# Performance work log

Hardware: AMD Instinct MI355X
Metric: run time of the kernel (lower is better)

The kernel has to match this reference:

```python
import jax, jax.numpy as jnp
import numpy as np

N_NODES = 10000
N_EDGES = 640000
D = 128


def setup_inputs() -> dict:
    key = jax.random.key(0)
    ks = jax.random.split(key, 8)
    x = jax.random.normal(ks[0], (N_NODES, D), dtype=jnp.float32)
    edge_weight = jax.random.uniform(ks[1], (N_EDGES,), dtype=jnp.float32)
    W0 = jax.random.normal(ks[2], (D, D), dtype=jnp.float32) * (1.0 / np.sqrt(D))
    b0 = jnp.zeros((D,), dtype=jnp.float32)
    W1 = jax.random.normal(ks[3], (D, D), dtype=jnp.float32) * (1.0 / np.sqrt(D))
    b1 = jnp.zeros((D,), dtype=jnp.float32)
    src = jax.random.randint(ks[4], (N_EDGES,), 0, N_NODES)
    dst = jax.random.randint(ks[5], (N_EDGES,), 0, N_NODES)
    return {"x": x, "edge_weight": edge_weight, "W0": W0, "b0": b0,
            "W1": W1, "b1": b1, "src": src, "dst": dst}


def _graph_conv(h, src, dst, edge_weight, W, b):
    # DGL GraphConv with norm='both', bias, activation=relu.
    n = h.shape[0]
    ones = jnp.ones((src.shape[0],), dtype=h.dtype)
    out_deg = jax.ops.segment_sum(ones, src, num_segments=n)
    in_deg = jax.ops.segment_sum(ones, dst, num_segments=n)
    norm_src = jax.lax.rsqrt(jnp.maximum(out_deg, 1.0))  # [N]
    norm_dst = jax.lax.rsqrt(jnp.maximum(in_deg, 1.0))   # [N]
    h = h * norm_src[:, None]
    # gather -> weight edges -> scatter-add (sparse neighbor aggregation)
    msg = h[src] * edge_weight[:, None]                  # [E, D]
    agg = jax.ops.segment_sum(msg, dst, num_segments=n)  # [N, D]
    rst = agg @ W                                        # in_feats == out_feats: aggregate first
    rst = rst * norm_dst[:, None] + b
    return jax.nn.relu(rst)  # activation inside GraphConv


def reference(x, edge_weight, W0, b0, W1, b1, src, dst):
    # NET.forward (full-graph path): per layer GraphConv -> activation -> dropout.
    # Dropout is identity in eval mode; outer relu after GraphConv's internal relu is idempotent
    # but applied for faithfulness.
    h = jax.nn.relu(_graph_conv(x, src, dst, edge_weight, W0, b0))
    h = jax.nn.relu(_graph_conv(h, src, dst, edge_weight, W1, b1))
    return h  # predict is None (n_classes=None)
```

## Files before the change

kernel.cpp:

```cpp
#include <hip/hip_runtime.h>
#include <hip/hip_fp16.h>

#define D 128
#define NB 256
#define Q 8
#define BQ (NB / Q)
#define NBINS_MAX 10016
#define GM 32

__global__ __launch_bounds__(256) void hist_kernel(const int* __restrict__ src, const int* __restrict__ dst,
                                                   const float* __restrict__ x, __half* __restrict__ xh, int total4,
                                                   int* __restrict__ pd, unsigned short* __restrict__ ps,
                                                   int E, int n) {
    __shared__ __align__(16) int hd[NBINS_MAX];
    __shared__ __align__(16) int hs[NBINS_MAX];
    int b = blockIdx.x, t = threadIdx.x;
    for (int i = b * 256 + t; i < total4; i += NB * 256) {
        float4 v = *(const float4*)(x + (size_t)i * 4);
        __half2 a = __floats2half2_rn(v.x, v.y);
        __half2 c = __floats2half2_rn(v.z, v.w);
        *(__half2*)(xh + (size_t)i * 4) = a;
        *(__half2*)(xh + (size_t)i * 4 + 2) = c;
    }
    int chunk = (E + NB - 1) / NB;
    int e0 = b * chunk, e1 = min(e0 + chunk, E);
    int nq = (n + 3) >> 2;
    for (int i = t; i < nq; i += 256) {
        *(int4*)(&hd[i * 4]) = make_int4(0, 0, 0, 0);
        *(int4*)(&hs[i * 4]) = make_int4(0, 0, 0, 0);
    }
    __syncthreads();
    for (int e = e0 + t; e < e1; e += 256) {
        atomicAdd(&hd[dst[e]], 1);
        atomicAdd(&hs[src[e]], 1);
    }
    __syncthreads();
    int nf = n >> 2;
    for (int i = t; i < nf; i += 256) {
        int4 h = *(const int4*)(&hd[i * 4]);
        *(int4*)(pd + (size_t)b * n + i * 4) = h;
        int4 s = *(const int4*)(&hs[i * 4]);
        uint2 u;
        u.x = (unsigned)(s.x & 0xFFFF) | ((unsigned)(s.y & 0xFFFF) << 16);
        u.y = (unsigned)(s.z & 0xFFFF) | ((unsigned)(s.w & 0xFFFF) << 16);
        *(uint2*)(ps + (size_t)b * n + i * 4) = u;
    }
    for (int i = nf * 4 + t; i < n; i += 256) {
        pd[(size_t)b * n + i] = hd[i];
        ps[(size_t)b * n + i] = (unsigned short)hs[i];
    }
}

__global__ __launch_bounds__(256) void colscan_kernel(int* __restrict__ pd, const unsigned short* __restrict__ ps,
                                                      int* __restrict__ qtot_d, int* __restrict__ qtot_s, int n) {
    int bin4 = (blockIdx.x * 256 + threadIdx.x) * 4;
    int q = blockIdx.y;
    if (bin4 >= n) return;
    int b0 = q * BQ;
    if (bin4 + 3 < n) {
        int4 run = make_int4(0, 0, 0, 0);
        int4 ssum = make_int4(0, 0, 0, 0);
#pragma unroll 8
        for (int j = 0; j < BQ; ++j) {
            size_t idx = (size_t)(b0 + j) * n + bin4;
            int4 v = *(const int4*)(pd + idx);
            *(int4*)(pd + idx) = run;
            run.x += v.x; run.y += v.y; run.z += v.z; run.w += v.w;
            uint2 u = *(const uint2*)(ps + idx);
            ssum.x += (int)(u.x & 0xFFFF); ssum.y += (int)(u.x >> 16);
            ssum.z += (int)(u.y & 0xFFFF); ssum.w += (int)(u.y >> 16);
        }
        *(int4*)(qtot_d + (size_t)q * n + bin4) = run;
        *(int4*)(qtot_s + (size_t)q * n + bin4) = ssum;
    } else {
        for (int bin = bin4; bin < n; ++bin) {
            int run = 0, ssum = 0;
            for (int j = 0; j < BQ; ++j) {
                size_t idx = (size_t)(b0 + j) * n + bin;
                int v = pd[idx];
                pd[idx] = run;
                run += v;
                ssum += (int)ps[idx];
            }
            qtot_d[(size_t)q * n + bin] = run;
            qtot_s[(size_t)q * n + bin] = ssum;
        }
    }
}

__global__ __launch_bounds__(1024) void finscan_kernel(int* __restrict__ qtot_d, const int* __restrict__ qtot_s,
                                                       int* __restrict__ row_start,
                                                       float* __restrict__ norm_src, float* __restrict__ norm_dst,
                                                       int n) {
    __shared__ int deg[NBINS_MAX];
    __shared__ int part[1024];
    int t = threadIdx.x;
    for (int b4 = t * 4; b4 < n; b4 += 4096) {
        if (b4 + 3 < n) {
            int4 qv[Q];
#pragma unroll
            for (int q = 0; q < Q; ++q) qv[q] = *(const int4*)(qtot_d + (size_t)q * n + b4);
            int4 run = make_int4(0, 0, 0, 0);
#pragma unroll
            for (int q = 0; q < Q; ++q) {
                *(int4*)(qtot_d + (size_t)q * n + b4) = run;
                run.x += qv[q].x; run.y += qv[q].y; run.z += qv[q].z; run.w += qv[q].w;
            }
            *(int4*)(&deg[b4]) = run;
            norm_dst[b4 + 0] = rsqrtf(fmaxf((float)run.x, 1.0f));
            norm_dst[b4 + 1] = rsqrtf(fmaxf((float)run.y, 1.0f));
            norm_dst[b4 + 2] = rsqrtf(fmaxf((float)run.z, 1.0f));
            norm_dst[b4 + 3] = rsqrtf(fmaxf((float)run.w, 1.0f));
            int4 st = make_int4(0, 0, 0, 0);
#pragma unroll
            for (int q = 0; q < Q; ++q) {
                int4 v = *(const int4*)(qtot_s + (size_t)q * n + b4);
                st.x += v.x; st.y += v.y; st.z += v.z; st.w += v.w;
            }
            norm_src[b4 + 0] = rsqrtf(fmaxf((float)st.x, 1.0f));
            norm_src[b4 + 1] = rsqrtf(fmaxf((float)st.y, 1.0f));
            norm_src[b4 + 2] = rsqrtf(fmaxf((float)st.z, 1.0f));
            norm_src[b4 + 3] = rsqrtf(fmaxf((float)st.w, 1.0f));
        } else {
            for (int bin = b4; bin < n; ++bin) {
                int run = 0;
                for (int q = 0; q < Q; ++q) {
                    size_t i = (size_t)q * n + bin;
                    int v = qtot_d[i];
                    qtot_d[i] = run;
                    run += v;
                }
                deg[bin] = run;
                norm_dst[bin] = rsqrtf(fmaxf((float)run, 1.0f));
                int tot = 0;
                for (int q = 0; q < Q; ++q) tot += qtot_s[(size_t)q * n + bin];
                norm_src[bin] = rsqrtf(fmaxf((float)tot, 1.0f));
            }
        }
    }
    __syncthreads();
    int ipt = (n + 1023) / 1024;
    int lo = min(t * ipt, n), hi = min(lo + ipt, n);
    int s = 0;
    for (int i = lo; i < hi; ++i) s += deg[i];
    part[t] = s;
    __syncthreads();
    for (int off = 1; off < 1024; off <<= 1) {
        int v = 0;
        if (t >= off) v = part[t - off];
        __syncthreads();
        if (t >= off) part[t] += v;
        __syncthreads();
    }
    int run = part[t] - s;
    for (int i = lo; i < hi; ++i) {
        int v = deg[i];
        row_start[i] = run;
        run += v;
    }
    if (t == 1023) row_start[n] = part[1023];
}

__global__ __launch_bounds__(256) void fill_kernel(const int* __restrict__ src, const int* __restrict__ dst,
                                                   const float* __restrict__ ew, const float* __restrict__ ns,
                                                   const int* __restrict__ row_start, const int* __restrict__ qbase,
                                                   const int* __restrict__ pd,
                                                   int2* __restrict__ sorted, int E, int n) {
    __shared__ __align__(16) int cursor[NBINS_MAX];
    int b = blockIdx.x, t = threadIdx.x;
    int q = b / BQ;
    int chunk = (E + NB - 1) / NB;
    int e0 = b * chunk, e1 = min(e0 + chunk, E);
    int nf = n >> 2;
    for (int i = t; i < nf; i += 256) {
        int4 r = *(const int4*)(row_start + i * 4);
        int4 a = *(const int4*)(qbase + (size_t)q * n + i * 4);
        int4 c = *(const int4*)(pd + (size_t)b * n + i * 4);
        *(int4*)(&cursor[i * 4]) = make_int4(r.x + a.x + c.x, r.y + a.y + c.y,
                                             r.z + a.z + c.z, r.w + a.w + c.w);
    }
    for (int i = nf * 4 + t; i < n; i += 256)
        cursor[i] = row_start[i] + qbase[(size_t)q * n + i] + pd[(size_t)b * n + i];
    __syncthreads();
    for (int e = e0 + t; e < e1; e += 256) {
        int d = dst[e];
        int slot = atomicAdd(&cursor[d], 1);
        int s = src[e];
        int2 rec;
        rec.x = s;
        rec.y = __float_as_int(ew[e] * ns[s]);
        sorted[slot] = rec;
    }
}

template <int EPI>
__global__ __launch_bounds__(256) void agg_kernel(const __half* __restrict__ h, const int* __restrict__ row_start,
                                                  const int2* __restrict__ sorted, float* __restrict__ out,
                                                  const float* __restrict__ norm_dst, const float* __restrict__ bias,
                                                  int n) {
    int wave = threadIdx.x >> 6;
    int lane = threadIdx.x & 63;
    int node = blockIdx.x * 4 + wave;
    if (node >= n) return;
    const __half2* hc = (const __half2*)h + lane;
    int beg = __builtin_amdgcn_readfirstlane(row_start[node]);
    int end = __builtin_amdgcn_readfirstlane(row_start[node + 1]);
    float accx = 0.f, accy = 0.f;
    int s = beg;
    if (s < end && (s & 1)) {
        int2 rr = sorted[s];
        float w = __int_as_float(rr.y);
        float2 f = __half22float2(hc[(size_t)rr.x << 6]);
        accx = fmaf(w, f.x, accx); accy = fmaf(w, f.y, accy);
        ++s;
    }
    int4 p0, p1, p2, p3, p4, p5, p6, p7;
    if (s + 16 <= end) {
        p0 = *(const int4*)(sorted + s);
        p1 = *(const int4*)(sorted + s + 2);
        p2 = *(const int4*)(sorted + s + 4);
        p3 = *(const int4*)(sorted + s + 6);
        p4 = *(const int4*)(sorted + s + 8);
        p5 = *(const int4*)(sorted + s + 10);
        p6 = *(const int4*)(sorted + s + 12);
        p7 = *(const int4*)(sorted + s + 14);
    }
    for (; s + 32 <= end; s += 16) {
        int4 q0 = *(const int4*)(sorted + s + 16);
        int4 q1 = *(const int4*)(sorted + s + 18);
        int4 q2 = *(const int4*)(sorted + s + 20);
        int4 q3 = *(const int4*)(sorted + s + 22);
        int4 q4 = *(const int4*)(sorted + s + 24);
        int4 q5 = *(const int4*)(sorted + s + 26);
        int4 q6 = *(const int4*)(sorted + s + 28);
        int4 q7 = *(const int4*)(sorted + s + 30);
        __half2 x0  = hc[(size_t)p0.x << 6];
        __half2 x1  = hc[(size_t)p0.z << 6];
        __half2 x2  = hc[(size_t)p1.x << 6];
        __half2 x3  = hc[(size_t)p1.z << 6];
        __half2 x4  = hc[(size_t)p2.x << 6];
        __half2 x5  = hc[(size_t)p2.z << 6];
        __half2 x6  = hc[(size_t)p3.x << 6];
        __half2 x7  = hc[(size_t)p3.z << 6];
        __half2 x8  = hc[(size_t)p4.x << 6];
        __half2 x9  = hc[(size_t)p4.z << 6];
        __half2 x10 = hc[(size_t)p5.x << 6];
        __half2 x11 = hc[(size_t)p5.z << 6];
        __half2 x12 = hc[(size_t)p6.x << 6];
        __half2 x13 = hc[(size_t)p6.z << 6];
        __half2 x14 = hc[(size_t)p7.x << 6];
        __half2 x15 = hc[(size_t)p7.z << 6];
        float2 f;
        f = __half22float2(x0);  accx = fmaf(__int_as_float(p0.y), f.x, accx); accy = fmaf(__int_as_float(p0.y), f.y, accy);
        f = __half22float2(x1);  accx = fmaf(__int_as_float(p0.w), f.x, accx); accy = fmaf(__int_as_float(p0.w), f.y, accy);
        f = __half22float2(x2);  accx = fmaf(__int_as_float(p1.y), f.x, accx); accy = fmaf(__int_as_float(p1.y), f.y, accy);
        f = __half22float2(x3);  accx = fmaf(__int_as_float(p1.w), f.x, accx); accy = fmaf(__int_as_float(p1.w), f.y, accy);
        f = __half22float2(x4);  accx = fmaf(__int_as_float(p2.y), f.x, accx); accy = fmaf(__int_as_float(p2.y), f.y, accy);
        f = __half22float2(x5);  accx = fmaf(__int_as_float(p2.w), f.x, accx); accy = fmaf(__int_as_float(p2.w), f.y, accy);
        f = __half22float2(x6);  accx = fmaf(__int_as_float(p3.y), f.x, accx); accy = fmaf(__int_as_float(p3.y), f.y, accy);
        f = __half22float2(x7);  accx = fmaf(__int_as_float(p3.w), f.x, accx); accy = fmaf(__int_as_float(p3.w), f.y, accy);
        f = __half22float2(x8);  accx = fmaf(__int_as_float(p4.y), f.x, accx); accy = fmaf(__int_as_float(p4.y), f.y, accy);
        f = __half22float2(x9);  accx = fmaf(__int_as_float(p4.w), f.x, accx); accy = fmaf(__int_as_float(p4.w), f.y, accy);
        f = __half22float2(x10); accx = fmaf(__int_as_float(p5.y), f.x, accx); accy = fmaf(__int_as_float(p5.y), f.y, accy);
        f = __half22float2(x11); accx = fmaf(__int_as_float(p5.w), f.x, accx); accy = fmaf(__int_as_float(p5.w), f.y, accy);
        f = __half22float2(x12); accx = fmaf(__int_as_float(p6.y), f.x, accx); accy = fmaf(__int_as_float(p6.y), f.y, accy);
        f = __half22float2(x13); accx = fmaf(__int_as_float(p6.w), f.x, accx); accy = fmaf(__int_as_float(p6.w), f.y, accy);
        f = __half22float2(x14); accx = fmaf(__int_as_float(p7.y), f.x, accx); accy = fmaf(__int_as_float(p7.y), f.y, accy);
        f = __half22float2(x15); accx = fmaf(__int_as_float(p7.w), f.x, accx); accy = fmaf(__int_as_float(p7.w), f.y, accy);
        p0 = q0; p1 = q1; p2 = q2; p3 = q3;
        p4 = q4; p5 = q5; p6 = q6; p7 = q7;
    }
    if (s + 16 <= end) {
        float2 f;
        f = __half22float2(hc[(size_t)p0.x << 6]); accx = fmaf(__int_as_float(p0.y), f.x, accx); accy = fmaf(__int_as_float(p0.y), f.y, accy);
        f = __half22float2(hc[(size_t)p0.z << 6]); accx = fmaf(__int_as_float(p0.w), f.x, accx); accy = fmaf(__int_as_float(p0.w), f.y, accy);
        f = __half22float2(hc[(size_t)p1.x << 6]); accx = fmaf(__int_as_float(p1.y), f.x, accx); accy = fmaf(__int_as_float(p1.y), f.y, accy);
        f = __half22float2(hc[(size_t)p1.z << 6]); accx = fmaf(__int_as_float(p1.w), f.x, accx); accy = fmaf(__int_as_float(p1.w), f.y, accy);
        f = __half22float2(hc[(size_t)p2.x << 6]); accx = fmaf(__int_as_float(p2.y), f.x, accx); accy = fmaf(__int_as_float(p2.y), f.y, accy);
        f = __half22float2(hc[(size_t)p2.z << 6]); accx = fmaf(__int_as_float(p2.w), f.x, accx); accy = fmaf(__int_as_float(p2.w), f.y, accy);
        f = __half22float2(hc[(size_t)p3.x << 6]); accx = fmaf(__int_as_float(p3.y), f.x, accx); accy = fmaf(__int_as_float(p3.y), f.y, accy);
        f = __half22float2(hc[(size_t)p3.z << 6]); accx = fmaf(__int_as_float(p3.w), f.x, accx); accy = fmaf(__int_as_float(p3.w), f.y, accy);
        f = __half22float2(hc[(size_t)p4.x << 6]); accx = fmaf(__int_as_float(p4.y), f.x, accx); accy = fmaf(__int_as_float(p4.y), f.y, accy);
        f = __half22float2(hc[(size_t)p4.z << 6]); accx = fmaf(__int_as_float(p4.w), f.x, accx); accy = fmaf(__int_as_float(p4.w), f.y, accy);
        f = __half22float2(hc[(size_t)p5.x << 6]); accx = fmaf(__int_as_float(p5.y), f.x, accx); accy = fmaf(__int_as_float(p5.y), f.y, accy);
        f = __half22float2(hc[(size_t)p5.z << 6]); accx = fmaf(__int_as_float(p5.w), f.x, accx); accy = fmaf(__int_as_float(p5.w), f.y, accy);
        f = __half22float2(hc[(size_t)p6.x << 6]); accx = fmaf(__int_as_float(p6.y), f.x, accx); accy = fmaf(__int_as_float(p6.y), f.y, accy);
        f = __half22float2(hc[(size_t)p6.z << 6]); accx = fmaf(__int_as_float(p6.w), f.x, accx); accy = fmaf(__int_as_float(p6.w), f.y, accy);
        f = __half22float2(hc[(size_t)p7.x << 6]); accx = fmaf(__int_as_float(p7.y), f.x, accx); accy = fmaf(__int_as_float(p7.y), f.y, accy);
        f = __half22float2(hc[(size_t)p7.z << 6]); accx = fmaf(__int_as_float(p7.w), f.x, accx); accy = fmaf(__int_as_float(p7.w), f.y, accy);
        s += 16;
    }
    if (s + 8 <= end) {
        int4 a0 = *(const int4*)(sorted + s);
        int4 a1 = *(const int4*)(sorted + s + 2);
        int4 a2 = *(const int4*)(sorted + s + 4);
        int4 a3 = *(const int4*)(sorted + s + 6);
        float2 f;
        f = __half22float2(hc[(size_t)a0.x << 6]); accx = fmaf(__int_as_float(a0.y), f.x, accx); accy = fmaf(__int_as_float(a0.y), f.y, accy);
        f = __half22float2(hc[(size_t)a0.z << 6]); accx = fmaf(__int_as_float(a0.w), f.x, accx); accy = fmaf(__int_as_float(a0.w), f.y, accy);
        f = __half22float2(hc[(size_t)a1.x << 6]); accx = fmaf(__int_as_float(a1.y), f.x, accx); accy = fmaf(__int_as_float(a1.y), f.y, accy);
        f = __half22float2(hc[(size_t)a1.z << 6]); accx = fmaf(__int_as_float(a1.w), f.x, accx); accy = fmaf(__int_as_float(a1.w), f.y, accy);
        f = __half22float2(hc[(size_t)a2.x << 6]); accx = fmaf(__int_as_float(a2.y), f.x, accx); accy = fmaf(__int_as_float(a2.y), f.y, accy);
        f = __half22float2(hc[(size_t)a2.z << 6]); accx = fmaf(__int_as_float(a2.w), f.x, accx); accy = fmaf(__int_as_float(a2.w), f.y, accy);
        f = __half22float2(hc[(size_t)a3.x << 6]); accx = fmaf(__int_as_float(a3.y), f.x, accx); accy = fmaf(__int_as_float(a3.y), f.y, accy);
        f = __half22float2(hc[(size_t)a3.z << 6]); accx = fmaf(__int_as_float(a3.w), f.x, accx); accy = fmaf(__int_as_float(a3.w), f.y, accy);
        s += 8;
    }
    for (; s + 2 <= end; s += 2) {
        int4 p = *(const int4*)(sorted + s);
        float2 f;
        f = __half22float2(hc[(size_t)p.x << 6]); accx = fmaf(__int_as_float(p.y), f.x, accx); accy = fmaf(__int_as_float(p.y), f.y, accy);
        f = __half22float2(hc[(size_t)p.z << 6]); accx = fmaf(__int_as_float(p.w), f.x, accx); accy = fmaf(__int_as_float(p.w), f.y, accy);
    }
    if (s < end) {
        int2 rr = sorted[s];
        float w = __int_as_float(rr.y);
        float2 f = __half22float2(hc[(size_t)rr.x << 6]);
        accx = fmaf(w, f.x, accx); accy = fmaf(w, f.y, accy);
    }
    float2 o;
    if (EPI) {
        float nd = norm_dst[node];
        o.x = fmaxf(fmaf(accx, nd, bias[lane * 2]), 0.f);
        o.y = fmaxf(fmaf(accy, nd, bias[lane * 2 + 1]), 0.f);
    } else {
        o.x = accx; o.y = accy;
    }
    *(float2*)(out + ((size_t)node << 7) + lane * 2) = o;
}

__global__ __launch_bounds__(256) void gemmfused_kernel(const float* __restrict__ A,
                                                        const float* __restrict__ W0, const float* __restrict__ b0,
                                                        const float* __restrict__ W1,
                                                        const float* __restrict__ norm_dst,
                                                        __half* __restrict__ out_h, int n) {
    __shared__ __align__(16) float sAT[D][GM + 2];
    int tid = threadIdx.x;
    int row0 = blockIdx.x * GM;
    for (int i = tid; i < GM * 32; i += 256) {
        int r = i >> 5;
        int kq = i & 31;
        int rr = row0 + r;
        float4 v = make_float4(0.f, 0.f, 0.f, 0.f);
        if (rr < n) v = *(const float4*)(A + (size_t)rr * D + kq * 4);
        sAT[kq * 4 + 0][r] = v.x;
        sAT[kq * 4 + 1][r] = v.y;
        sAT[kq * 4 + 2][r] = v.z;
        sAT[kq * 4 + 3][r] = v.w;
    }
    __syncthreads();
    int tx = tid & 15;
    int ty = tid >> 4;
    int c0 = tx * 8;
    int r0 = ty * 2;
    float acc0[8], acc1[8];
#pragma unroll
    for (int j = 0; j < 8; ++j) { acc0[j] = 0.f; acc1[j] = 0.f; }
    {
        const float* Wk = W0 + c0;
#pragma unroll 4
        for (int k = 0; k < D; ++k) {
            float2 a = *(const float2*)&sAT[k][r0];
            float4 w0 = *(const float4*)(Wk);
            float4 w1 = *(const float4*)(Wk + 4);
            Wk += D;
            acc0[0] = fmaf(a.x, w0.x, acc0[0]);
            acc0[1] = fmaf(a.x, w0.y, acc0[1]);
            acc0[2] = fmaf(a.x, w0.z, acc0[2]);
            acc0[3] = fmaf(a.x, w0.w, acc0[3]);
            acc0[4] = fmaf(a.x, w1.x, acc0[4]);
            acc0[5] = fmaf(a.x, w1.y, acc0[5]);
            acc0[6] = fmaf(a.x, w1.z, acc0[6]);
            acc0[7] = fmaf(a.x, w1.w, acc0[7]);
            acc1[0] = fmaf(a.y, w0.x, acc1[0]);
            acc1[1] = fmaf(a.y, w0.y, acc1[1]);
            acc1[2] = fmaf(a.y, w0.z, acc1[2]);
            acc1[3] = fmaf(a.y, w0.w, acc1[3]);
            acc1[4] = fmaf(a.y, w1.x, acc1[4]);
            acc1[5] = fmaf(a.y, w1.y, acc1[5]);
            acc1[6] = fmaf(a.y, w1.z, acc1[6]);
            acc1[7] = fmaf(a.y, w1.w, acc1[7]);
        }
    }
    __syncthreads();
#pragma unroll 2
    for (int rr = 0; rr < 2; ++rr) {
        int r = row0 + r0 + rr;
        if (r >= n) continue;
        float* acc = rr ? acc1 : acc0;
        float nd = norm_dst[r];
#pragma unroll
        for (int j = 0; j < 8; ++j)
            sAT[c0 + j][r0 + rr] = fmaxf(fmaf(acc[j], nd, b0[c0 + j]), 0.f);
    }
    __syncthreads();
#pragma unroll
    for (int j = 0; j < 8; ++j) { acc0[j] = 0.f; acc1[j] = 0.f; }
    {
        const float* Wk = W1 + c0;
#pragma unroll 4
        for (int k = 0; k < D; ++k) {
            float2 a = *(const float2*)&sAT[k][r0];
            float4 w0 = *(const float4*)(Wk);
            float4 w1 = *(const float4*)(Wk + 4);
            Wk += D;
            acc0[0] = fmaf(a.x, w0.x, acc0[0]);
            acc0[1] = fmaf(a.x, w0.y, acc0[1]);
            acc0[2] = fmaf(a.x, w0.z, acc0[2]);
            acc0[3] = fmaf(a.x, w0.w, acc0[3]);
            acc0[4] = fmaf(a.x, w1.x, acc0[4]);
            acc0[5] = fmaf(a.x, w1.y, acc0[5]);
            acc0[6] = fmaf(a.x, w1.z, acc0[6]);
            acc0[7] = fmaf(a.x, w1.w, acc0[7]);
            acc1[0] = fmaf(a.y, w0.x, acc1[0]);
            acc1[1] = fmaf(a.y, w0.y, acc1[1]);
            acc1[2] = fmaf(a.y, w0.z, acc1[2]);
            acc1[3] = fmaf(a.y, w0.w, acc1[3]);
            acc1[4] = fmaf(a.y, w1.x, acc1[4]);
            acc1[5] = fmaf(a.y, w1.y, acc1[5]);
            acc1[6] = fmaf(a.y, w1.z, acc1[6]);
            acc1[7] = fmaf(a.y, w1.w, acc1[7]);
        }
    }
#pragma unroll 2
    for (int rr = 0; rr < 2; ++rr) {
        int r = row0 + r0 + rr;
        if (r >= n) continue;
        float* acc = rr ? acc1 : acc0;
        __half2 h0 = __floats2half2_rn(acc[0], acc[1]);
        __half2 h1 = __floats2half2_rn(acc[2], acc[3]);
        __half2 h2 = __floats2half2_rn(acc[4], acc[5]);
        __half2 h3 = __floats2half2_rn(acc[6], acc[7]);
        __half* p = out_h + (size_t)r * D + c0;
        *(__half2*)(p + 0) = h0;
        *(__half2*)(p + 2) = h1;
        *(__half2*)(p + 4) = h2;
        *(__half2*)(p + 6) = h3;
    }
}

extern "C" void kernel_launch(void* const* d_in, const int* in_sizes, int n_in,
                              void* d_out, int out_size, void* d_ws, size_t ws_size,
                              hipStream_t stream) {
    const float* x  = (const float*)d_in[0];
    const float* ew = (const float*)d_in[1];
    const float* W0 = (const float*)d_in[2];
    const float* b0 = (const float*)d_in[3];
    const float* W1 = (const float*)d_in[4];
    const float* b1 = (const float*)d_in[5];
    const int* src  = (const int*)d_in[6];
    const int* dst  = (const int*)d_in[7];
    float* out = (float*)d_out;

    int n = in_sizes[0] / D;
    int E = in_sizes[6];
    if (n <= 0 || E <= 0) return;

    char* ws = (char*)d_ws;
    size_t off = 0;
    auto alloc = [&](size_t bytes) -> void* {
        void* p = ws + off;
        off = (off + bytes + 255) & ~(size_t)255;
        return p;
    };
    int* row_start  = (int*)alloc(((size_t)n + 1) * 4);
    float* norm_src = (float*)alloc((size_t)n * 4);
    float* norm_dst = (float*)alloc((size_t)n * 4);
    int* qtot_d     = (int*)alloc((size_t)Q * n * 4);
    int* qtot_s     = (int*)alloc((size_t)Q * n * 4);
    int2* sorted    = (int2*)alloc((size_t)E * 8);
    int* pd         = (int*)alloc((size_t)NB * n * 4);
    unsigned short* ps = (unsigned short*)alloc((size_t)NB * n * 2);
    float* B1       = (float*)alloc((size_t)n * D * 4);
    __half* xh      = (__half*)alloc((size_t)n * D * 2);
    __half* th      = (__half*)alloc((size_t)n * D * 2);

    int nb4 = (n + 1023) / 1024;
    int ab = (n + 3) / 4;
    int gb = (n + GM - 1) / GM;

    hist_kernel<<<NB, 256, 0, stream>>>(src, dst, x, xh, n * D / 4, pd, ps, E, n);
    colscan_kernel<<<dim3(nb4, Q), 256, 0, stream>>>(pd, ps, qtot_d, qtot_s, n);
    finscan_kernel<<<1, 1024, 0, stream>>>(qtot_d, qtot_s, row_start, norm_src, norm_dst, n);
    fill_kernel<<<NB, 256, 0, stream>>>(src, dst, ew, norm_src, row_start, qtot_d, pd, sorted, E, n);

    agg_kernel<0><<<ab, 256, 0, stream>>>(xh, row_start, sorted, B1, nullptr, nullptr, n);
    gemmfused_kernel<<<gb, 256, 0, stream>>>(B1, W0, b0, W1, norm_dst, th, n);
    agg_kernel<1><<<ab, 256, 0, stream>>>(th, row_start, sorted, out, norm_dst, b1, n);
}
```

Baseline: 182.4 us.

## Fuse CSR preprocessing kernels into one persistent kernel with grid barriers

Merges the histogram, column-scan, final-scan and fill kernels into a single persistent kernel of NB blocks separated by software grid barriers built on atomic counters. The single-block 1024-thread final scan becomes a multi-block scan with per-block partial sums and a serial base computation. This is meant to remove three kernel launch gaps and the serial single-block scan bottleneck. It relies on all 256 blocks being co-resident, which large shared memory use makes a deadlock risk if occupancy is insufficient, and it adds a memset plus spin-wait costs.

```diff
diff --git a/kernel.cpp b/kernel.cpp
--- a/kernel.cpp
+++ b/kernel.cpp
@@ -8,13 +8,35 @@
 #define NBINS_MAX 10016
 #define GM 32
 
-__global__ __launch_bounds__(256) void hist_kernel(const int* __restrict__ src, const int* __restrict__ dst,
-                                                   const float* __restrict__ x, __half* __restrict__ xh, int total4,
-                                                   int* __restrict__ pd, unsigned short* __restrict__ ps,
-                                                   int E, int n) {
+__device__ __forceinline__ void gridbar(int* bar, int phase) {
+    __syncthreads();
+    if (threadIdx.x == 0) {
+        __threadfence();
+        atomicAdd(bar, 1);
+        int target = NB * (phase + 1);
+        while (atomicAdd(bar, 0) < target) { __builtin_amdgcn_s_sleep(2); }
+        __threadfence();
+    }
+    __syncthreads();
+}
+
+__global__ __launch_bounds__(256) void preprocess_kernel(
+        const int* __restrict__ src, const int* __restrict__ dst,
+        const float* __restrict__ x, __half* __restrict__ xh, int total4,
+        const float* __restrict__ ew,
+        int* __restrict__ pd, unsigned short* __restrict__ ps,
+        int* __restrict__ qtot_d, int* __restrict__ qtot_s,
+        int* __restrict__ row_start, float* __restrict__ norm_src, float* __restrict__ norm_dst,
+        int2* __restrict__ sorted,
+        int* __restrict__ bar, int* __restrict__ part_g, int* __restrict__ base_g,
+        int E, int n, int nb4) {
     __shared__ __align__(16) int hd[NBINS_MAX];
     __shared__ __align__(16) int hs[NBINS_MAX];
     int b = blockIdx.x, t = threadIdx.x;
+    int chunk = (E + NB - 1) / NB;
+    int e0 = b * chunk, e1 = min(e0 + chunk, E);
+    int nf = n >> 2;
+
     for (int i = b * 256 + t; i < total4; i += NB * 256) {
         float4 v = *(const float4*)(x + (size_t)i * 4);
         __half2 a = __floats2half2_rn(v.x, v.y);
@@ -22,8 +44,6 @@
         *(__half2*)(xh + (size_t)i * 4) = a;
         *(__half2*)(xh + (size_t)i * 4 + 2) = c;
     }
-    int chunk = (E + NB - 1) / NB;
-    int e0 = b * chunk, e1 = min(e0 + chunk, E);
     int nq = (n + 3) >> 2;
     for (int i = t; i < nq; i += 256) {
         *(int4*)(&hd[i * 4]) = make_int4(0, 0, 0, 0);
@@ -35,7 +55,6 @@
         atomicAdd(&hs[src[e]], 1);
     }
     __syncthreads();
-    int nf = n >> 2;
     for (int i = t; i < nf; i += 256) {
         int4 h = *(const int4*)(&hd[i * 4]);
         *(int4*)(pd + (size_t)b * n + i * 4) = h;
@@ -49,54 +68,55 @@
         pd[(size_t)b * n + i] = hd[i];
         ps[(size_t)b * n + i] = (unsigned short)hs[i];
     }
-}
-
-__global__ __launch_bounds__(256) void colscan_kernel(int* __restrict__ pd, const unsigned short* __restrict__ ps,
-                                                      int* __restrict__ qtot_d, int* __restrict__ qtot_s, int n) {
-    int bin4 = (blockIdx.x * 256 + threadIdx.x) * 4;
-    int q = blockIdx.y;
-    if (bin4 >= n) return;
-    int b0 = q * BQ;
-    if (bin4 + 3 < n) {
-        int4 run = make_int4(0, 0, 0, 0);
-        int4 ssum = make_int4(0, 0, 0, 0);
+    gridbar(bar, 0);
+
+    if (b < nb4 * Q) {
+        int gx = b % nb4;
+        int q  = b / nb4;
+        int bin4 = (gx * 256 + t) * 4;
+        if (bin4 < n) {
+            int b0 = q * BQ;
+            if (bin4 + 3 < n) {
+                int4 run = make_int4(0, 0, 0, 0);
+                int4 ssum = make_int4(0, 0, 0, 0);
 #pragma unroll 8
-        for (int j = 0; j < BQ; ++j) {
-            size_t idx = (size_t)(b0 + j) * n + bin4;
-            int4 v = *(const int4*)(pd + idx);
-            *(int4*)(pd + idx) = run;
-            run.x += v.x; run.y += v.y; run.z += v.z; run.w += v.w;
-            uint2 u = *(const uint2*)(ps + idx);
-            ssum.x += (int)(u.x & 0xFFFF); ssum.y += (int)(u.x >> 16);
-            ssum.z += (int)(u.y & 0xFFFF); ssum.w += (int)(u.y >> 16);
-        }
-        *(int4*)(qtot_d + (size_t)q * n + bin4) = run;
-        *(int4*)(qtot_s + (size_t)q * n + bin4) = ssum;
-    } else {
-        for (int bin = bin4; bin < n; ++bin) {
-            int run = 0, ssum = 0;
-            for (int j = 0; j < BQ; ++j) {
-                size_t idx = (size_t)(b0 + j) * n + bin;
-                int v = pd[idx];
-                pd[idx] = run;
-                run += v;
-                ssum += (int)ps[idx];
+                for (int j = 0; j < BQ; ++j) {
+                    size_t idx = (size_t)(b0 + j) * n + bin4;
+                    int4 v = *(const int4*)(pd + idx);
+                    *(int4*)(pd + idx) = run;
+                    run.x += v.x; run.y += v.y; run.z += v.z; run.w += v.w;
+                    uint2 u = *(const uint2*)(ps + idx);
+                    ssum.x += (int)(u.x & 0xFFFF); ssum.y += (int)(u.x >> 16);
+                    ssum.z += (int)(u.y & 0xFFFF); ssum.w += (int)(u.y >> 16);
+                }
+                *(int4*)(qtot_d + (size_t)q * n + bin4) = run;
+                *(int4*)(qtot_s + (size_t)q * n + bin4) = ssum;
+            } else {
+                for (int bin = bin4; bin < n; ++bin) {
+                    int run = 0, ssum = 0;
+                    for (int j = 0; j < BQ; ++j) {
+                        size_t idx = (size_t)(b0 + j) * n + bin;
+                        int v = pd[idx];
+                        pd[idx] = run;
+                        run += v;
+                        ssum += (int)ps[idx];
+                    }
+                    qtot_d[(size_t)q * n + bin] = run;
+                    qtot_s[(size_t)q * n + bin] = ssum;
+                }
             }
-            qtot_d[(size_t)q * n + bin] = run;
-            qtot_s[(size_t)q * n + bin] = ssum;
-        }
-    }
-}
-
-__global__ __launch_bounds__(1024) void finscan_kernel(int* __restrict__ qtot_d, const int* __restrict__ qtot_s,
-                                                       int* __restrict__ row_start,
-                                                       float* __restrict__ norm_src, float* __restrict__ norm_dst,
-                                                       int n) {
-    __shared__ int deg[NBINS_MAX];
-    __shared__ int part[1024];
-    int t = threadIdx.x;
-    for (int b4 = t * 4; b4 < n; b4 += 4096) {
-        if (b4 + 3 < n) {
+        }
+    }
+    gridbar(bar, 1);
+
+    int* degL = hs;
+    int* redL = hd;
+    if (b < nb4) {
+        int l4 = t * 4;
+        int b4 = b * 1024 + l4;
+        int cnt = (b4 < n) ? min(4, n - b4) : 0;
+        int tot = 0;
+        if (cnt == 4) {
             int4 qv[Q];
 #pragma unroll
             for (int q = 0; q < Q; ++q) qv[q] = *(const int4*)(qtot_d + (size_t)q * n + b4);
@@ -106,7 +126,7 @@
                 *(int4*)(qtot_d + (size_t)q * n + b4) = run;
                 run.x += qv[q].x; run.y += qv[q].y; run.z += qv[q].z; run.w += qv[q].w;
             }
-            *(int4*)(&deg[b4]) = run;
+            *(int4*)(&degL[l4]) = run;
             norm_dst[b4 + 0] = rsqrtf(fmaxf((float)run.x, 1.0f));
             norm_dst[b4 + 1] = rsqrtf(fmaxf((float)run.y, 1.0f));
             norm_dst[b4 + 2] = rsqrtf(fmaxf((float)run.z, 1.0f));
@@ -121,8 +141,10 @@
             norm_src[b4 + 1] = rsqrtf(fmaxf((float)st.y, 1.0f));
             norm_src[b4 + 2] = rsqrtf(fmaxf((float)st.z, 1.0f));
             norm_src[b4 + 3] = rsqrtf(fmaxf((float)st.w, 1.0f));
-        } else {
-            for (int bin = b4; bin < n; ++bin) {
+            tot = run.x + run.y + run.z + run.w;
+        } else if (cnt > 0) {
+            for (int j = 0; j < cnt; ++j) {
+                int bin = b4 + j;
                 int run = 0;
                 for (int q = 0; q < Q; ++q) {
                     size_t i = (size_t)q * n + bin;
@@ -130,66 +152,78 @@
                     qtot_d[i] = run;
                     run += v;
                 }
-                deg[bin] = run;
+                degL[l4 + j] = run;
+                tot += run;
                 norm_dst[bin] = rsqrtf(fmaxf((float)run, 1.0f));
-                int tot = 0;
-                for (int q = 0; q < Q; ++q) tot += qtot_s[(size_t)q * n + bin];
-                norm_src[bin] = rsqrtf(fmaxf((float)tot, 1.0f));
+                int tt = 0;
+                for (int q = 0; q < Q; ++q) tt += qtot_s[(size_t)q * n + bin];
+                norm_src[bin] = rsqrtf(fmaxf((float)tt, 1.0f));
             }
         }
-    }
-    __syncthreads();
-    int ipt = (n + 1023) / 1024;
-    int lo = min(t * ipt, n), hi = min(lo + ipt, n);
-    int s = 0;
-    for (int i = lo; i < hi; ++i) s += deg[i];
-    part[t] = s;
-    __syncthreads();
-    for (int off = 1; off < 1024; off <<= 1) {
-        int v = 0;
-        if (t >= off) v = part[t - off];
+        redL[t] = tot;
         __syncthreads();
-        if (t >= off) part[t] += v;
+        for (int off = 128; off > 0; off >>= 1) {
+            if (t < off) redL[t] += redL[t + off];
+            __syncthreads();
+        }
+        if (t == 0) part_g[b] = redL[0];
+    }
+    gridbar(bar, 2);
+
+    if (b == 0 && t == 0) {
+        int running = 0;
+        for (int i = 0; i < nb4; ++i) {
+            base_g[i] = running;
+            running += part_g[i];
+        }
+        row_start[n] = running;
+    }
+    gridbar(bar, 3);
+
+    if (b < nb4) {
+        int l4 = t * 4;
+        int b4 = b * 1024 + l4;
+        int cnt = (b4 < n) ? min(4, n - b4) : 0;
+        int tot = 0;
+        for (int j = 0; j < cnt; ++j) tot += degL[l4 + j];
+        redL[t] = tot;
         __syncthreads();
-    }
-    int run = part[t] - s;
-    for (int i = lo; i < hi; ++i) {
-        int v = deg[i];
-        row_start[i] = run;
-        run += v;
-    }
-    if (t == 1023) row_start[n] = part[1023];
-}
-
-__global__ __launch_bounds__(256) void fill_kernel(const int* __restrict__ src, const int* __restrict__ dst,
-                                                   const float* __restrict__ ew, const float* __restrict__ ns,
-                                                   const int* __restrict__ row_start, const int* __restrict__ qbase,
-                                                   const int* __restrict__ pd,
-                                                   int2* __restrict__ sorted, int E, int n) {
-    __shared__ __align__(16) int cursor[NBINS_MAX];
-    int b = blockIdx.x, t = threadIdx.x;
-    int q = b / BQ;
-    int chunk = (E + NB - 1) / NB;
-    int e0 = b * chunk, e1 = min(e0 + chunk, E);
-    int nf = n >> 2;
-    for (int i = t; i < nf; i += 256) {
-        int4 r = *(const int4*)(row_start + i * 4);
-        int4 a = *(const int4*)(qbase + (size_t)q * n + i * 4);
-        int4 c = *(const int4*)(pd + (size_t)b * n + i * 4);
-        *(int4*)(&cursor[i * 4]) = make_int4(r.x + a.x + c.x, r.y + a.y + c.y,
-                                             r.z + a.z + c.z, r.w + a.w + c.w);
-    }
-    for (int i = nf * 4 + t; i < n; i += 256)
-        cursor[i] = row_start[i] + qbase[(size_t)q * n + i] + pd[(size_t)b * n + i];
-    __syncthreads();
-    for (int e = e0 + t; e < e1; e += 256) {
-        int d = dst[e];
-        int slot = atomicAdd(&cursor[d], 1);
-        int s = src[e];
-        int2 rec;
-        rec.x = s;
-        rec.y = __float_as_int(ew[e] * ns[s]);
-        sorted[slot] = rec;
+        for (int off = 1; off < 256; off <<= 1) {
+            int v = (t >= off) ? redL[t - off] : 0;
+            __syncthreads();
+            if (t >= off) redL[t] += v;
+            __syncthreads();
+        }
+        int run = base_g[b] + redL[t] - tot;
+        for (int j = 0; j < cnt; ++j) {
+            row_start[b4 + j] = run;
+            run += degL[l4 + j];
+        }
+    }
+    gridbar(bar, 4);
+
+    {
+        int* cursor = hd;
+        int q = b / BQ;
+        for (int i = t; i < nf; i += 256) {
+            int4 r = *(const int4*)(row_start + i * 4);
+            int4 a = *(const int4*)(qtot_d + (size_t)q * n + i * 4);
+            int4 c = *(const int4*)(pd + (size_t)b * n + i * 4);
+            *(int4*)(&cursor[i * 4]) = make_int4(r.x + a.x + c.x, r.y + a.y + c.y,
+                                                 r.z + a.z + c.z, r.w + a.w + c.w);
+        }
+        for (int i = nf * 4 + t; i < n; i += 256)
+            cursor[i] = row_start[i] + qtot_d[(size_t)q * n + i] + pd[(size_t)b * n + i];
+        __syncthreads();
+        for (int e = e0 + t; e < e1; e += 256) {
+            int d = dst[e];
+            int slot = atomicAdd(&cursor[d], 1);
+            int s = src[e];
+            int2 rec;
+            rec.x = s;
+            rec.y = __float_as_int(ew[e] * norm_src[s]);
+            sorted[slot] = rec;
+        }
     }
 }
 
@@ -474,15 +508,19 @@
     float* B1       = (float*)alloc((size_t)n * D * 4);
     __half* xh      = (__half*)alloc((size_t)n * D * 2);
     __half* th      = (__half*)alloc((size_t)n * D * 2);
+    int* bar        = (int*)alloc(256);
+    int* part_g     = (int*)alloc(64 * 4);
+    int* base_g     = (int*)alloc(64 * 4);
 
     int nb4 = (n + 1023) / 1024;
     int ab = (n + 3) / 4;
     int gb = (n + GM - 1) / GM;
 
-    hist_kernel<<<NB, 256, 0, stream>>>(src, dst, x, xh, n * D / 4, pd, ps, E, n);
-    colscan_kernel<<<dim3(nb4, Q), 256, 0, stream>>>(pd, ps, qtot_d, qtot_s, n);
-    finscan_kernel<<<1, 1024, 0, stream>>>(qtot_d, qtot_s, row_start, norm_src, norm_dst, n);
-    fill_kernel<<<NB, 256, 0, stream>>>(src, dst, ew, norm_src, row_start, qtot_d, pd, sorted, E, n);
+    hipMemsetAsync(bar, 0, 4, stream);
+    preprocess_kernel<<<NB, 256, 0, stream>>>(src, dst, x, xh, n * D / 4, ew,
+                                              pd, ps, qtot_d, qtot_s,
+                                              row_start, norm_src, norm_dst, sorted,
+                                              bar, part_g, base_g, E, n, nb4);
 
     agg_kernel<0><<<ab, 256, 0, stream>>>(xh, row_start, sorted, B1, nullptr, nullptr, n);
     gemmfused_kernel<<<gb, 256, 0, stream>>>(B1, W0, b0, W1, norm_dst, th, n);
```

New measurement: 258.4 us. 1.42x slower.
